# Kernel tuning notes

Hardware: AMD Instinct MI355X
Metric: run time of the kernel (lower is better)

Reference implementation:

```python
import jax, jax.numpy as jnp
import numpy as np

B, S, E, H = 4, 1024, 1024, 16
HD = E // H
MAX_SEQ = 5000


def setup_inputs() -> dict:
    key = jax.random.key(0)
    ks = jax.random.split(key, 10)
    def lin(kw, kb):
        w = jax.random.normal(kw, (E, E), dtype=jnp.float32) * (1.0 / np.sqrt(E))
        b = jax.random.normal(kb, (E,), dtype=jnp.float32) * 0.01
        return w, b
    wq, bq = lin(ks[0], ks[1])
    wk, bk = lin(ks[2], ks[3])
    wv, bv = lin(ks[4], ks[5])
    wo, bo = lin(ks[6], ks[7])
    rpe_table = jax.random.normal(ks[8], (H, 2 * MAX_SEQ - 1, HD), dtype=jnp.float32) * 0.02
    x = jax.random.normal(ks[9], (B, S, E), dtype=jnp.float32)
    return {"x": x, "wq": wq, "bq": bq, "wk": wk, "bk": bk,
            "wv": wv, "bv": bv, "wo": wo, "bo": bo, "rpe_table": rpe_table}


def reference(x, wq, bq, wk, bk, wv, bv, wo, bo, rpe_table):
    b, s, e = x.shape
    scale = 1.0 / np.sqrt(HD)
    # projections (torch Linear: y = x @ W^T + b), reshape to (b, h, s, hd)
    q = (x @ wq.T + bq).reshape(b, s, H, HD).transpose(0, 2, 1, 3)
    k = (x @ wk.T + bk).reshape(b, s, H, HD).transpose(0, 2, 1, 3)
    v = (x @ wv.T + bv).reshape(b, s, H, HD).transpose(0, 2, 1, 3)
    scores = jnp.einsum('bhqd,bhkd->bhqk', q, k) * scale
    # RPE: rpe[h, q, k, d] = table[h, q - k + s - 1, d]; factor the einsum:
    # rel[b,h,q,r] = sum_d q[b,h,q,d] * table[h,r,d], then gather r = q - k + s - 1
    table = rpe_table[:, : 2 * s - 1]               # (H, 2s-1, HD)
    rel = jnp.einsum('bhqd,hrd->bhqr', q, table)    # (b, H, s, 2s-1)
    idx = jnp.arange(s)[:, None] - jnp.arange(s)[None, :] + (s - 1)  # (s, s)
    rpe_scores = jnp.take_along_axis(
        rel, jnp.broadcast_to(idx[None, None], (b, H, s, s)), axis=-1)
    attn = jax.nn.softmax(scores + rpe_scores, axis=-1)
    ctx = jnp.einsum('bhqk,bhkd->bhqd', attn, v)
    ctx = ctx.transpose(0, 2, 1, 3).reshape(b, s, e)
    return ctx @ wo.T + bo
```

## Files before the change

kernel.cpp:

```cpp
#include <hip/hip_runtime.h>
#include <hip/hip_bf16.h>
#include <stdint.h>

typedef __attribute__((ext_vector_type(8))) short s8v;
typedef __attribute__((ext_vector_type(4))) float f32x4;
typedef __attribute__((ext_vector_type(16))) float f32x16;

union V16 { uint4 u4; unsigned int u[4]; s8v s; };

__device__ inline s8v u4_to_s8(uint4 v) { V16 c; c.u4 = v; return c.s; }
__device__ inline s8v words_to_s8(unsigned int a, unsigned int b, unsigned int c, unsigned int d) {
  V16 t; t.u[0] = a; t.u[1] = b; t.u[2] = c; t.u[3] = d; return t.s;
}
__device__ inline unsigned short f2b(float f) {
  __hip_bfloat16 h = __float2bfloat16(f);
  unsigned short u; __builtin_memcpy(&u, &h, 2); return u;
}
__device__ inline unsigned int pack2(float lo, float hi) {
  return ((unsigned int)f2b(hi) << 16) | (unsigned int)f2b(lo);
}
__device__ inline unsigned int cvtpk(float lo, float hi) {
  unsigned int r; asm("v_cvt_pk_bf16_f32 %0, %1, %2" : "=v"(r) : "v"(lo), "v"(hi)); return r;
}
__device__ inline float exp2_fast(float x) {
#if __has_builtin(__builtin_amdgcn_exp2f)
  return __builtin_amdgcn_exp2f(x);
#else
  float y; asm("v_exp_f32 %0, %1" : "=v"(y) : "v"(x)); return y;
#endif
}
__device__ inline void gld16(const void* g, void* lds) {
  __builtin_amdgcn_global_load_lds((const __attribute__((address_space(1))) void*)g,
                                   (__attribute__((address_space(3))) void*)lds, 16, 0, 0);
}

#define LOG2E 1.4426950408889634f

__global__ void cvt_xw_kernel(const float* __restrict__ x, const float* __restrict__ wq,
                              const float* __restrict__ wk, const float* __restrict__ wv,
                              const float* __restrict__ wo,
                              __hip_bfloat16* __restrict__ XB, __hip_bfloat16* __restrict__ WQKV,
                              __hip_bfloat16* __restrict__ WOb) {
  size_t i = ((size_t)blockIdx.x * 256 + threadIdx.x) * 8;
  const float* src; __hip_bfloat16* dst; size_t off;
  if (i < 4194304)      { src = x;  dst = XB;             off = i; }
  else if (i < 5242880) { src = wq; dst = WQKV;           off = i - 4194304; }
  else if (i < 6291456) { src = wk; dst = WQKV + 1048576; off = i - 5242880; }
  else if (i < 7340032) { src = wv; dst = WQKV + 2097152; off = i - 6291456; }
  else                  { src = wo; dst = WOb;            off = i - 7340032; }
  const float4* s4 = (const float4*)(src + off);
  float4 a = s4[0], b = s4[1];
  uint4 o;
  o.x = pack2(a.x, a.y); o.y = pack2(a.z, a.w);
  o.z = pack2(b.x, b.y); o.w = pack2(b.z, b.w);
  *(uint4*)(dst + off) = o;
}

__global__ __launch_bounds__(256, 3) void gemm_qkv(
    const __hip_bfloat16* __restrict__ A,
    const __hip_bfloat16* __restrict__ Bt,
    const float* __restrict__ bq, const float* __restrict__ bk, const float* __restrict__ bv,
    __hip_bfloat16* __restrict__ QB, __hip_bfloat16* __restrict__ KB,
    __hip_bfloat16* __restrict__ VTB,
    const float* __restrict__ tb, __hip_bfloat16* __restrict__ TBL) {
  const int flat = blockIdx.x;
  if (flat >= 768) {
    size_t i = ((size_t)(flat - 768) * 256 + threadIdx.x) * 8;
    int h = (int)(i >> 17);
    int rem = (int)(i & 131071);
    int r = rem >> 6, c = rem & 63;
    uint4 o;
    if (r < 2047) {
      const float4* s4 = (const float4*)(tb + ((size_t)h * 9999 + r) * 64 + c);
      float4 a = s4[0], b = s4[1];
      o.x = pack2(a.x * LOG2E, a.y * LOG2E); o.y = pack2(a.z * LOG2E, a.w * LOG2E);
      o.z = pack2(b.x * LOG2E, b.y * LOG2E); o.w = pack2(b.z * LOG2E, b.w * LOG2E);
    } else { o.x = 0u; o.y = 0u; o.z = 0u; o.w = 0u; }
    *(uint4*)(TBL + i) = o;
    return;
  }

  __shared__ __align__(16) char smem[32768];
  char* As = smem;
  char* Bs = smem + 16384;
  const int tid = threadIdx.x;
  const int w = tid >> 6, l = tid & 63;
  const int wr = w >> 1, wc = w & 1;
  const int lr = l & 15, lg = l >> 4;
  const int wg = (flat & 7) * 96 + (flat >> 3);
  const int nt = wg % 24, mt = wg / 24;
  const int m0 = mt * 128, n0 = nt * 128;

  f32x4 acc[4][4] = {};

  for (int kt = 0; kt < 16; ++kt) {
    __syncthreads();
    #pragma unroll
    for (int i = 0; i < 4; ++i) {
      const int off = i * 4096 + w * 1024;
      const int loff = off + l * 16;
      const int row = loff >> 7;
      const int cb = loff & 127;
      const int sc = cb ^ ((row & 7) << 4);
      gld16((const char*)A  + (size_t)(m0 + row) * 2048 + kt * 128 + sc, As + off);
      gld16((const char*)Bt + (size_t)(n0 + row) * 2048 + kt * 128 + sc, Bs + off);
    }
    asm volatile("s_waitcnt vmcnt(0)" ::: "memory");
    __syncthreads();
    #pragma unroll
    for (int ks = 0; ks < 2; ++ks) {
      uint4 af[4], bf4[4];
      #pragma unroll
      for (int i = 0; i < 4; ++i) {
        const int ra = wr * 64 + i * 16 + lr;
        const int rb = wc * 64 + i * 16 + lr;
        const int cb = ks * 64 + lg * 16;
        af[i]  = *(const uint4*)(As + ra * 128 + (cb ^ ((ra & 7) << 4)));
        bf4[i] = *(const uint4*)(Bs + rb * 128 + (cb ^ ((rb & 7) << 4)));
      }
      #pragma unroll
      for (int i = 0; i < 4; ++i) {
        #pragma unroll
        for (int j = 0; j < 4; ++j)
          acc[i][j] = __builtin_amdgcn_mfma_f32_16x16x32_bf16(u4_to_s8(af[i]), u4_to_s8(bf4[j]), acc[i][j], 0, 0, 0);
      }
    }
  }

  const int mrow = m0 + wr * 64 + lg * 4;
  const int ncol = n0 + wc * 64 + lr;
  const int cls = nt >> 3;

  if (cls < 2) {
    const float sc = cls ? 0.125f * LOG2E : 1.0f;
    const float* bias = cls ? bk : bq;
    __hip_bfloat16* op = cls ? KB : QB;
    #pragma unroll
    for (int j = 0; j < 4; ++j) {
      const int n = ncol - cls * 1024 + j * 16;
      const float bia = bias[n];
      const int hh = n >> 6, hd = n & 63;
      #pragma unroll
      for (int i = 0; i < 4; ++i) {
        #pragma unroll
        for (int r = 0; r < 4; ++r) {
          const int m = mrow + i * 16 + r;
          const int bb = m >> 10, ss = m & 1023;
          op[(((size_t)(bb * 16 + hh)) * 1024 + ss) * 64 + hd] = __float2bfloat16((acc[i][j][r] + bia) * sc);
        }
      }
    }
  } else {
    #pragma unroll
    for (int j = 0; j < 4; ++j) {
      const int f = ncol - 2048 + j * 16;
      const float bia = bv[f];
      const int fh = f >> 6, fd = f & 63;
      #pragma unroll
      for (int i = 0; i < 4; ++i) {
        const int m = mrow + i * 16;
        const int bb = m >> 10, ss = m & 1023;
        ushort4 qv;
        qv.x = f2b(acc[i][j][0] + bia); qv.y = f2b(acc[i][j][1] + bia);
        qv.z = f2b(acc[i][j][2] + bia); qv.w = f2b(acc[i][j][3] + bia);
        *(ushort4*)((char*)VTB + (((size_t)bb * 1048576 + (size_t)fh * 65536 + fd * 1024 + ss) * 2)) = qv;
      }
    }
  }
}

__global__ __launch_bounds__(256, 3) void gemm_out(
    const __hip_bfloat16* __restrict__ A,
    const __hip_bfloat16* __restrict__ Bt,
    const float* __restrict__ bo,
    float* __restrict__ out) {
  __shared__ __align__(16) char smem[24576];
  char* As = smem;
  char* Bs = smem + 16384;
  const int tid = threadIdx.x;
  const int w = tid >> 6, l = tid & 63;
  const int wr = w >> 1, wc = w & 1;
  const int lr = l & 15, lg = l >> 4;
  const int flat = blockIdx.x;
  const int wg = (flat & 7) * 64 + (flat >> 3);
  const int nt = wg & 15, mt = wg >> 4;
  const int m0 = mt * 128, n0 = nt * 64;

  f32x4 acc[4][2] = {};

  for (int kt = 0; kt < 16; ++kt) {
    __syncthreads();
    #pragma unroll
    for (int i = 0; i < 4; ++i) {
      const int off = i * 4096 + w * 1024;
      const int loff = off + l * 16;
      const int row = loff >> 7;
      const int cb = loff & 127;
      const int sc = cb ^ ((row & 7) << 4);
      gld16((const char*)A + (size_t)(m0 + row) * 2048 + kt * 128 + sc, As + off);
    }
    #pragma unroll
    for (int i = 0; i < 2; ++i) {
      const int off = i * 4096 + w * 1024;
      const int loff = off + l * 16;
      const int row = loff >> 7;
      const int cb = loff & 127;
      const int sc = cb ^ ((row & 7) << 4);
      gld16((const char*)Bt + (size_t)(n0 + row) * 2048 + kt * 128 + sc, Bs + off);
    }
    asm volatile("s_waitcnt vmcnt(0)" ::: "memory");
    __syncthreads();
    #pragma unroll
    for (int ks = 0; ks < 2; ++ks) {
      uint4 af[4], bf2[2];
      #pragma unroll
      for (int i = 0; i < 4; ++i) {
        const int ra = wr * 64 + i * 16 + lr;
        const int cb = ks * 64 + lg * 16;
        af[i] = *(const uint4*)(As + ra * 128 + (cb ^ ((ra & 7) << 4)));
      }
      #pragma unroll
      for (int j = 0; j < 2; ++j) {
        const int rb = wc * 32 + j * 16 + lr;
        const int cb = ks * 64 + lg * 16;
        bf2[j] = *(const uint4*)(Bs + rb * 128 + (cb ^ ((rb & 7) << 4)));
      }
      #pragma unroll
      for (int i = 0; i < 4; ++i) {
        #pragma unroll
        for (int j = 0; j < 2; ++j)
          acc[i][j] = __builtin_amdgcn_mfma_f32_16x16x32_bf16(u4_to_s8(af[i]), u4_to_s8(bf2[j]), acc[i][j], 0, 0, 0);
      }
    }
  }

  const int mrow = m0 + wr * 64 + lg * 4;
  const int ncol = n0 + wc * 32 + lr;
  #pragma unroll
  for (int j = 0; j < 2; ++j) {
    const int n = ncol + j * 16;
    const float bia = bo[n];
    #pragma unroll
    for (int i = 0; i < 4; ++i) {
      #pragma unroll
      for (int r = 0; r < 4; ++r) {
        const int m = mrow + i * 16 + r;
        out[(size_t)m * 1024 + n] = acc[i][j][r] + bia;
      }
    }
  }
}

__global__ __launch_bounds__(256, 2) void attn_kernel(
    const __hip_bfloat16* __restrict__ Qg,
    const __hip_bfloat16* __restrict__ Kg,
    const __hip_bfloat16* __restrict__ VTg,
    const __hip_bfloat16* __restrict__ Tg,
    __hip_bfloat16* __restrict__ Cg) {
  __shared__ __align__(16) char smem[65536];
  char* Klds = smem;
  char* Tlds = smem + 8192;
  const int tid = threadIdx.x;
  const int w = tid >> 6, l = tid & 63;
  const int ql = l & 31, half = l >> 5;
  char* relw = smem + 32768 + w * 8192;

  const int bx = blockIdx.x;
  const int work = (bx & 7) * 64 + (bx >> 3);
  const int b = work & 3, hqt = work >> 2;
  const int h = hqt >> 3, qt = hqt & 7;
  const int qb = qt * 128;
  const int q0 = qb + 32 * w;

  const size_t bh = (size_t)(b * 16 + h);
  const char* Qb = (const char*)Qg + bh * 131072;
  const char* Kb = (const char*)Kg + bh * 131072;
  const char* Vb = (const char*)VTg + bh * 131072;
  const char* Tb = (const char*)Tg + (size_t)h * 262144;

  const int relsw = ql * 256 + ((ql & 15) << 4);
  const int u4 = (ql << 2) - (half << 4);
  const int k0sw = ql * 128 + ((ql & 7) << 4);
  const int k1sw = (32 + ql) * 128 + ((ql & 7) << 4);

  auto stageK = [&](int k0n) {
    #pragma unroll
    for (int i = 0; i < 2; ++i) {
      const int loff = i * 4096 + w * 1024 + l * 16;
      const int row = loff >> 7, cb = loff & 127;
      const int sc = cb ^ ((row & 7) << 4);
      gld16(Kb + (size_t)(k0n + row) * 128 + sc, Klds + i * 4096 + w * 1024);
    }
  };
  auto stageT = [&](int rsrc) {
    const int slot = (int)(((unsigned)(rsrc >> 6)) % 3u);
    char* dst = Tlds + slot * 8192;
    #pragma unroll
    for (int i = 0; i < 2; ++i) {
      const int loff = i * 4096 + w * 1024 + l * 16;
      const int row = loff >> 7, cb = loff & 127;
      const int sc = cb ^ ((row & 7) << 4);
      gld16(Tb + (size_t)(rsrc + row) * 128 + sc, dst + i * 4096 + w * 1024);
    }
  };

  s8v qv[4];
  {
    const char* qrow = Qb + (size_t)(q0 + ql) * 128 + half * 16;
    #pragma unroll
    for (int ds = 0; ds < 4; ++ds) qv[ds] = u4_to_s8(*(const uint4*)(qrow + ds * 32));
  }

  f32x16 cacc0 = {}, cacc1 = {};
  f32x16 rcache = {};
  float mL = -1.0e30f, lsum = 0.0f;
  int rbase = qb + 960;

  for (int kt = 0; kt < 16; ++kt, rbase -= 64) {
    __syncthreads();
    stageK(kt * 64);
    stageT(rbase);
    if (kt == 0) { stageT(rbase + 64); stageT(rbase + 128); }
    asm volatile("s_waitcnt vmcnt(0)" ::: "memory");
    __syncthreads();

    uint4 vr[8];
    { const int kn = kt * 128;
      #pragma unroll
      for (int t = 0; t < 2; ++t)
        #pragma unroll
        for (int ks = 0; ks < 4; ++ks)
          vr[t * 4 + ks] = *(const uint4*)(Vb + (size_t)(t * 32 + ql) * 2048 + kn + ks * 32 + half * 16);
    }

    auto relTile = [&](int bt) {
      const int slot = (int)(((unsigned)(rbase >> 6) + (unsigned)((w + bt) >> 1)) % 3u);
      const int rowin = ((w + bt) & 1) * 32 + ql;
      const int tbsw = slot * 8192 + rowin * 128 + ((ql & 7) << 4);
      f32x16 racc = {};
      __builtin_amdgcn_s_setprio(1);
      #pragma unroll
      for (int ds = 0; ds < 4; ++ds) {
        const int cb = ds * 32 + half * 16;
        uint4 tf = *(const uint4*)(Tlds + (tbsw ^ cb));
        racc = __builtin_amdgcn_mfma_f32_32x32x16_bf16(u4_to_s8(tf), qv[ds], racc, 0, 0, 0);
      }
      __builtin_amdgcn_s_setprio(0);
      return racc;
    };

    f32x16 racc2 = (kt == 0) ? relTile(2) : rcache;
    #pragma unroll
    for (int g = 0; g < 4; ++g)
      #pragma unroll
      for (int j = 0; j < 4; ++j) {
        const int pos4 = (u4 + 4 * (-1 - j - 8 * g)) & 124;
        *(float*)(relw + (relsw ^ pos4)) = racc2[4 * g + j];
      }
    f32x16 racc0 = relTile(0);
    #pragma unroll
    for (int g = 0; g < 4; ++g)
      #pragma unroll
      for (int j = 0; j < 4; ++j) {
        const int pos4 = ((u4 + 4 * (63 - j - 8 * g)) & 252) | 128;
        *(float*)(relw + (relsw ^ pos4)) = racc0[4 * g + j];
      }
    rcache = racc0;
    f32x16 racc1 = relTile(1);
    #pragma unroll
    for (int g = 0; g < 4; ++g)
      #pragma unroll
      for (int j = 0; j < 4; ++j) {
        const int pos4 = (u4 + 4 * (31 - j - 8 * g)) & 252;
        *(float*)(relw + (relsw ^ pos4)) = racc1[4 * g + j];
      }

    f32x16 p0 = {}, p1 = {};
    __builtin_amdgcn_s_setprio(1);
    #pragma unroll
    for (int ds = 0; ds < 4; ++ds) {
      const int cb = ds * 32 + half * 16;
      uint4 kf0 = *(const uint4*)(Klds + (k0sw ^ cb));
      uint4 kf1 = *(const uint4*)(Klds + (k1sw ^ cb));
      p0 = __builtin_amdgcn_mfma_f32_32x32x16_bf16(u4_to_s8(kf0), qv[ds], p0, 0, 0, 0);
      p1 = __builtin_amdgcn_mfma_f32_32x32x16_bf16(u4_to_s8(kf1), qv[ds], p1, 0, 0, 0);
    }
    __builtin_amdgcn_s_setprio(0);

    #pragma unroll
    for (int mp = 0; mp < 4; ++mp) {
      const int X0 = 32 * mp + 16 * half;
      f32x4 r0 = *(const f32x4*)(relw + (relsw ^ X0));
      f32x4 r1 = *(const f32x4*)(relw + (relsw ^ (X0 + 128)));
      #pragma unroll
      for (int j = 0; j < 4; ++j) {
        p0[4 * mp + j] += r0[j];
        p1[4 * mp + j] += r1[j];
      }
    }

    float mx[8];
    #pragma unroll
    for (int i = 0; i < 8; ++i)
      mx[i] = fmaxf(fmaxf(p0[2 * i], p0[2 * i + 1]), fmaxf(p1[2 * i], p1[2 * i + 1]));
    float pmax = fmaxf(fmaxf(fmaxf(mx[0], mx[1]), fmaxf(mx[2], mx[3])),
                       fmaxf(fmaxf(mx[4], mx[5]), fmaxf(mx[6], mx[7])));
    pmax = fmaxf(pmax, __shfl_xor(pmax, 32));
    if (!__all(pmax - mL <= 12.0f)) {
      const float mnew = fmaxf(mL, pmax);
      const float corr = exp2_fast(mL - mnew);
      mL = mnew;
      lsum *= corr;
      #pragma unroll
      for (int r = 0; r < 16; ++r) {
        const float cr = __shfl(corr, (r & 3) + 8 * (r >> 2) + 4 * half);
        cacc0[r] *= cr;
        cacc1[r] *= cr;
      }
    }
    #pragma unroll
    for (int r = 0; r < 16; ++r) {
      p0[r] = exp2_fast(p0[r] - mL);
      p1[r] = exp2_fast(p1[r] - mL);
    }
    float sm[8];
    #pragma unroll
    for (int i = 0; i < 8; ++i)
      sm[i] = (p0[2 * i] + p0[2 * i + 1]) + (p1[2 * i] + p1[2 * i + 1]);
    float psum = ((sm[0] + sm[1]) + (sm[2] + sm[3])) + ((sm[4] + sm[5]) + (sm[6] + sm[7]));
    psum += __shfl_xor(psum, 32);
    lsum += psum;

    unsigned int w0[8], w1[8];
    #pragma unroll
    for (int jw = 0; jw < 8; ++jw) {
      w0[jw] = cvtpk(p0[2 * jw], p0[2 * jw + 1]);
      w1[jw] = cvtpk(p1[2 * jw], p1[2 * jw + 1]);
    }
    unsigned int r0x[4], r1x[4];
    #pragma unroll
    for (int i = 0; i < 4; ++i) {
      const int jkeep = (i & 1) + 4 * (i >> 1);
      const int jsend = jkeep + 2;
      unsigned int v0 = half ? w0[jkeep] : w0[jsend];
      unsigned int v1 = half ? w1[jkeep] : w1[jsend];
      r0x[i] = (unsigned int)__shfl_xor((int)v0, 32);
      r1x[i] = (unsigned int)__shfl_xor((int)v1, 32);
    }

    __builtin_amdgcn_s_setprio(1);
    #pragma unroll
    for (int ks = 0; ks < 4; ++ks) {
      const int mm = ks & 1;
      unsigned int f0_, f1_, f2_, f3_;
      if (ks < 2) {
        f0_ = half ? r0x[2 * mm]     : w0[4 * mm];
        f1_ = half ? r0x[2 * mm + 1] : w0[4 * mm + 1];
        f2_ = half ? w0[4 * mm + 2]  : r0x[2 * mm];
        f3_ = half ? w0[4 * mm + 3]  : r0x[2 * mm + 1];
      } else {
        f0_ = half ? r1x[2 * mm]     : w1[4 * mm];
        f1_ = half ? r1x[2 * mm + 1] : w1[4 * mm + 1];
        f2_ = half ? w1[4 * mm + 2]  : r1x[2 * mm];
        f3_ = half ? w1[4 * mm + 3]  : r1x[2 * mm + 1];
      }
      s8v pf = words_to_s8(f0_, f1_, f2_, f3_);
      cacc0 = __builtin_amdgcn_mfma_f32_32x32x16_bf16(pf, u4_to_s8(vr[ks]), cacc0, 0, 0, 0);
      cacc1 = __builtin_amdgcn_mfma_f32_32x32x16_bf16(pf, u4_to_s8(vr[4 + ks]), cacc1, 0, 0, 0);
    }
    __builtin_amdgcn_s_setprio(0);
  }

  #pragma unroll
  for (int r = 0; r < 16; ++r) {
    const int qr = (r & 3) + 8 * (r >> 2) + 4 * half;
    const float inv = 1.0f / __shfl(lsum, qr);
    const size_t row = (size_t)b * 1024 + q0 + qr;
    const size_t basei = row * 1024 + h * 64 + ql;
    Cg[basei]      = __float2bfloat16(cacc0[r] * inv);
    Cg[basei + 32] = __float2bfloat16(cacc1[r] * inv);
  }
}

extern "C" void kernel_launch(void* const* d_in, const int* in_sizes, int n_in,
                              void* d_out, int out_size, void* d_ws, size_t ws_size,
                              hipStream_t stream) {
  (void)in_sizes; (void)n_in; (void)out_size; (void)ws_size;
  const float* x  = (const float*)d_in[0];
  const float* wq = (const float*)d_in[1];
  const float* bq = (const float*)d_in[2];
  const float* wk = (const float*)d_in[3];
  const float* bk = (const float*)d_in[4];
  const float* wv = (const float*)d_in[5];
  const float* bv = (const float*)d_in[6];
  const float* wo = (const float*)d_in[7];
  const float* bo = (const float*)d_in[8];
  const float* tb = (const float*)d_in[9];

  char* ws = (char*)d_ws;
  __hip_bfloat16* XB   = (__hip_bfloat16*)(ws);
  __hip_bfloat16* WQKV = (__hip_bfloat16*)(ws + 8388608);
  __hip_bfloat16* WOb  = (__hip_bfloat16*)(ws + 14680064);
  __hip_bfloat16* TBL  = (__hip_bfloat16*)(ws + 16777216);
  __hip_bfloat16* QB   = (__hip_bfloat16*)(ws + 20971520);
  __hip_bfloat16* KB   = (__hip_bfloat16*)(ws + 29360128);
  __hip_bfloat16* VTB  = (__hip_bfloat16*)(ws + 37748736);
  __hip_bfloat16* CTX  = (__hip_bfloat16*)(ws + 46137344);

  cvt_xw_kernel<<<4096, 256, 0, stream>>>(x, wq, wk, wv, wo, XB, WQKV, WOb);
  gemm_qkv<<<1792, 256, 0, stream>>>(XB, WQKV, bq, bk, bv, QB, KB, VTB, tb, TBL);
  attn_kernel<<<512, 256, 0, stream>>>(QB, KB, VTB, TBL, CTX);
  gemm_out<<<512, 256, 0, stream>>>(CTX, WOb, bo, (float*)d_out);
}
```

Measured before the change: 105.0 us.

## Stage two K tiles per barrier in attention and shrink output GEMM tiles

```diff
diff --git a/kernel.cpp b/kernel.cpp
--- a/kernel.cpp
+++ b/kernel.cpp
@@ -169,36 +169,27 @@
   }
 }
 
-__global__ __launch_bounds__(256, 3) void gemm_out(
+__global__ __launch_bounds__(256, 4) void gemm_out(
     const __hip_bfloat16* __restrict__ A,
     const __hip_bfloat16* __restrict__ Bt,
     const float* __restrict__ bo,
     float* __restrict__ out) {
-  __shared__ __align__(16) char smem[24576];
+  __shared__ __align__(16) char smem[16384];
   char* As = smem;
-  char* Bs = smem + 16384;
+  char* Bs = smem + 8192;
   const int tid = threadIdx.x;
   const int w = tid >> 6, l = tid & 63;
   const int wr = w >> 1, wc = w & 1;
   const int lr = l & 15, lg = l >> 4;
   const int flat = blockIdx.x;
-  const int wg = (flat & 7) * 64 + (flat >> 3);
+  const int wg = (flat & 7) * 128 + (flat >> 3);
   const int nt = wg & 15, mt = wg >> 4;
-  const int m0 = mt * 128, n0 = nt * 64;
-
-  f32x4 acc[4][2] = {};
+  const int m0 = mt * 64, n0 = nt * 64;
+
+  f32x4 acc[2][2] = {};
 
   for (int kt = 0; kt < 16; ++kt) {
     __syncthreads();
-    #pragma unroll
-    for (int i = 0; i < 4; ++i) {
-      const int off = i * 4096 + w * 1024;
-      const int loff = off + l * 16;
-      const int row = loff >> 7;
-      const int cb = loff & 127;
-      const int sc = cb ^ ((row & 7) << 4);
-      gld16((const char*)A + (size_t)(m0 + row) * 2048 + kt * 128 + sc, As + off);
-    }
     #pragma unroll
     for (int i = 0; i < 2; ++i) {
       const int off = i * 4096 + w * 1024;
@@ -206,16 +197,17 @@
       const int row = loff >> 7;
       const int cb = loff & 127;
       const int sc = cb ^ ((row & 7) << 4);
+      gld16((const char*)A  + (size_t)(m0 + row) * 2048 + kt * 128 + sc, As + off);
       gld16((const char*)Bt + (size_t)(n0 + row) * 2048 + kt * 128 + sc, Bs + off);
     }
     asm volatile("s_waitcnt vmcnt(0)" ::: "memory");
     __syncthreads();
     #pragma unroll
     for (int ks = 0; ks < 2; ++ks) {
-      uint4 af[4], bf2[2];
-      #pragma unroll
-      for (int i = 0; i < 4; ++i) {
-        const int ra = wr * 64 + i * 16 + lr;
+      uint4 af[2], bf2[2];
+      #pragma unroll
+      for (int i = 0; i < 2; ++i) {
+        const int ra = wr * 32 + i * 16 + lr;
         const int cb = ks * 64 + lg * 16;
         af[i] = *(const uint4*)(As + ra * 128 + (cb ^ ((ra & 7) << 4)));
       }
@@ -226,7 +218,7 @@
         bf2[j] = *(const uint4*)(Bs + rb * 128 + (cb ^ ((rb & 7) << 4)));
       }
       #pragma unroll
-      for (int i = 0; i < 4; ++i) {
+      for (int i = 0; i < 2; ++i) {
         #pragma unroll
         for (int j = 0; j < 2; ++j)
           acc[i][j] = __builtin_amdgcn_mfma_f32_16x16x32_bf16(u4_to_s8(af[i]), u4_to_s8(bf2[j]), acc[i][j], 0, 0, 0);
@@ -234,14 +226,14 @@
     }
   }
 
-  const int mrow = m0 + wr * 64 + lg * 4;
+  const int mrow = m0 + wr * 32 + lg * 4;
   const int ncol = n0 + wc * 32 + lr;
   #pragma unroll
   for (int j = 0; j < 2; ++j) {
     const int n = ncol + j * 16;
     const float bia = bo[n];
     #pragma unroll
-    for (int i = 0; i < 4; ++i) {
+    for (int i = 0; i < 2; ++i) {
       #pragma unroll
       for (int r = 0; r < 4; ++r) {
         const int m = mrow + i * 16 + r;
@@ -257,13 +249,13 @@
     const __hip_bfloat16* __restrict__ VTg,
     const __hip_bfloat16* __restrict__ Tg,
     __hip_bfloat16* __restrict__ Cg) {
-  __shared__ __align__(16) char smem[65536];
+  __shared__ __align__(16) char smem[81920];
   char* Klds = smem;
-  char* Tlds = smem + 8192;
+  char* Tlds = smem + 16384;
   const int tid = threadIdx.x;
   const int w = tid >> 6, l = tid & 63;
   const int ql = l & 31, half = l >> 5;
-  char* relw = smem + 32768 + w * 8192;
+  char* relw = smem + 49152 + w * 8192;
 
   const int bx = blockIdx.x;
   const int work = (bx & 7) * 64 + (bx >> 3);
@@ -283,24 +275,23 @@
   const int k0sw = ql * 128 + ((ql & 7) << 4);
   const int k1sw = (32 + ql) * 128 + ((ql & 7) << 4);
 
-  auto stageK = [&](int k0n) {
+  auto stageK = [&](int k0n, int buf) {
     #pragma unroll
     for (int i = 0; i < 2; ++i) {
       const int loff = i * 4096 + w * 1024 + l * 16;
       const int row = loff >> 7, cb = loff & 127;
       const int sc = cb ^ ((row & 7) << 4);
-      gld16(Kb + (size_t)(k0n + row) * 128 + sc, Klds + i * 4096 + w * 1024);
+      gld16(Kb + (size_t)(k0n + row) * 128 + sc, Klds + buf * 8192 + i * 4096 + w * 1024);
     }
   };
-  auto stageT = [&](int rsrc) {
-    const int slot = (int)(((unsigned)(rsrc >> 6)) % 3u);
-    char* dst = Tlds + slot * 8192;
+  auto stageT = [&](int c) {
+    char* dst = Tlds + (c & 3) * 8192;
     #pragma unroll
     for (int i = 0; i < 2; ++i) {
       const int loff = i * 4096 + w * 1024 + l * 16;
       const int row = loff >> 7, cb = loff & 127;
       const int sc = cb ^ ((row & 7) << 4);
-      gld16(Tb + (size_t)(rsrc + row) * 128 + sc, dst + i * 4096 + w * 1024);
+      gld16(Tb + ((size_t)c * 64 + row) * 128 + sc, dst + i * 4096 + w * 1024);
     }
   };
 
@@ -314,15 +305,9 @@
   f32x16 cacc0 = {}, cacc1 = {};
   f32x16 rcache = {};
   float mL = -1.0e30f, lsum = 0.0f;
-  int rbase = qb + 960;
-
-  for (int kt = 0; kt < 16; ++kt, rbase -= 64) {
-    __syncthreads();
-    stageK(kt * 64);
-    stageT(rbase);
-    if (kt == 0) { stageT(rbase + 64); stageT(rbase + 128); }
-    asm volatile("s_waitcnt vmcnt(0)" ::: "memory");
-    __syncthreads();
+
+  auto computeKT = [&](int kt, int kbase) {
+    const int rbase = qb + 960 - 64 * kt;
 
     uint4 vr[8];
     { const int kn = kt * 128;
@@ -334,7 +319,7 @@
     }
 
     auto relTile = [&](int bt) {
-      const int slot = (int)(((unsigned)(rbase >> 6) + (unsigned)((w + bt) >> 1)) % 3u);
+      const int slot = ((rbase >> 6) + ((w + bt) >> 1)) & 3;
       const int rowin = ((w + bt) & 1) * 32 + ql;
       const int tbsw = slot * 8192 + rowin * 128 + ((ql & 7) << 4);
       f32x16 racc = {};
@@ -380,8 +365,8 @@
     #pragma unroll
     for (int ds = 0; ds < 4; ++ds) {
       const int cb = ds * 32 + half * 16;
-      uint4 kf0 = *(const uint4*)(Klds + (k0sw ^ cb));
-      uint4 kf1 = *(const uint4*)(Klds + (k1sw ^ cb));
+      uint4 kf0 = *(const uint4*)(Klds + kbase + (k0sw ^ cb));
+      uint4 kf1 = *(const uint4*)(Klds + kbase + (k1sw ^ cb));
       p0 = __builtin_amdgcn_mfma_f32_32x32x16_bf16(u4_to_s8(kf0), qv[ds], p0, 0, 0, 0);
       p1 = __builtin_amdgcn_mfma_f32_32x32x16_bf16(u4_to_s8(kf1), qv[ds], p1, 0, 0, 0);
     }
@@ -469,6 +454,26 @@
       cacc1 = __builtin_amdgcn_mfma_f32_32x32x16_bf16(pf, u4_to_s8(vr[4 + ks]), cacc1, 0, 0, 0);
     }
     __builtin_amdgcn_s_setprio(0);
+  };
+
+  const int c0 = (qb + 960) >> 6;
+  stageK(0, 0); stageK(64, 1);
+  stageT(c0 - 1); stageT(c0); stageT(c0 + 1); stageT(c0 + 2);
+  asm volatile("s_waitcnt vmcnt(0)" ::: "memory");
+  __syncthreads();
+
+  for (int s = 0; s < 8; ++s) {
+    computeKT(2 * s, 0);
+    computeKT(2 * s + 1, 8192);
+    __syncthreads();
+    if (s < 7) {
+      stageK((2 * s + 2) * 64, 0);
+      stageK((2 * s + 3) * 64, 1);
+      const int cn = (qb + 960 - 128 * (s + 1)) >> 6;
+      stageT(cn - 1); stageT(cn);
+      asm volatile("s_waitcnt vmcnt(0)" ::: "memory");
+    }
+    __syncthreads();
   }
 
   #pragma unroll
@@ -510,5 +515,5 @@
   cvt_xw_kernel<<<4096, 256, 0, stream>>>(x, wq, wk, wv, wo, XB, WQKV, WOb);
   gemm_qkv<<<1792, 256, 0, stream>>>(XB, WQKV, bq, bk, bv, QB, KB, VTB, tb, TBL);
   attn_kernel<<<512, 256, 0, stream>>>(QB, KB, VTB, TBL, CTX);
-  gemm_out<<<512, 256, 0, stream>>>(CTX, WOb, bo, (float*)d_out);
-}
+  gemm_out<<<1024, 256, 0, stream>>>(CTX, WOb, bo, (float*)d_out);
+}
```

After: 103.5 us (median of 2 runs). Within noise of the previous version (-1.5%).
